# Performance work log

Hardware: AMD Instinct MI355X
Metric: run time of the kernel (lower is better)

The kernel has to match this reference:

```python
import jax, jax.numpy as jnp
import numpy as np

B, N, D = 2, 2048, 1024   # batch, seq_len, d_model
E = 2 * D                  # d_inner = d_model * expand_factor
F = 4 * D                  # ffn hidden
CHUNK = 128
EPS_LN = 1e-5


def setup_inputs() -> dict:
    key = jax.random.key(0)
    ks = jax.random.split(key, 16)
    s = 0.02
    return {
        "x": jax.random.normal(ks[0], (B, N, D), dtype=jnp.float32),
        # linear-attention projections (stored [in, out])
        "q_w": jax.random.normal(ks[1], (D, E), dtype=jnp.float32) * s,
        "q_b": jnp.zeros((E,), jnp.float32),
        "k_w": jax.random.normal(ks[2], (D, E), dtype=jnp.float32) * s,
        "k_b": jnp.zeros((E,), jnp.float32),
        "v_w": jax.random.normal(ks[3], (D, E), dtype=jnp.float32) * s,
        "v_b": jnp.zeros((E,), jnp.float32),
        "o_w": jax.random.normal(ks[4], (E, D), dtype=jnp.float32) * s,
        "o_b": jnp.zeros((D,), jnp.float32),
        # layer norms
        "ln1_g": jnp.ones((D,), jnp.float32), "ln1_b": jnp.zeros((D,), jnp.float32),
        "ln2_g": jnp.ones((D,), jnp.float32), "ln2_b": jnp.zeros((D,), jnp.float32),
        # ffn
        "w1": jax.random.normal(ks[5], (D, F), dtype=jnp.float32) * s,
        "b1": jnp.zeros((F,), jnp.float32),
        "w2": jax.random.normal(ks[6], (F, D), dtype=jnp.float32) * s,
        "b2": jnp.zeros((D,), jnp.float32),
    }


def _layer_norm(x, g, b):
    mu = jnp.mean(x, axis=-1, keepdims=True)
    var = jnp.mean(jnp.square(x - mu), axis=-1, keepdims=True)
    return (x - mu) * jax.lax.rsqrt(var + EPS_LN) * g + b


def _feature_map(x):
    return jax.nn.elu(x) + 1.0  # positive features


def _causal_linear_attention(Q, K, V):
    """Exactly cumsum(k v^T) formulation, computed chunk-recurrently.
    Q,K: [B,N,E] (post feature map), V: [B,N,E]. Returns [B,N,E]."""
    nC = N // CHUNK
    Qc = Q.reshape(B, nC, CHUNK, E).transpose(1, 0, 2, 3)
    Kc = K.reshape(B, nC, CHUNK, E).transpose(1, 0, 2, 3)
    Vc = V.reshape(B, nC, CHUNK, E).transpose(1, 0, 2, 3)
    tril = jnp.tril(jnp.ones((CHUNK, CHUNK), Q.dtype))

    def step(S, qkv):  # S: [B,E,E] running sum of k v^T
        q, k, v = qkv
        scores = jnp.einsum('bcd,bkd->bck', q, k) * tril  # intra-chunk causal
        intra = jnp.einsum('bck,bke->bce', scores, v)
        inter = jnp.einsum('bcd,bde->bce', q, S)
        S = S + jnp.einsum('bcd,bce->bde', k, v)
        return S, intra + inter

    S0 = jnp.zeros((B, E, E), Q.dtype)
    _, num = jax.lax.scan(step, S0, (Qc, Kc, Vc))  # [nC,B,CHUNK,E]
    num = num.transpose(1, 0, 2, 3).reshape(B, N, E)
    Z = jnp.cumsum(K, axis=1)                       # [B,N,E]
    den = jnp.einsum('bnd,bnd->bn', Q, Z)[..., None] + 1e-6
    return num / den


def reference(x, q_w, q_b, k_w, k_b, v_w, v_b, o_w, o_b,
              ln1_g, ln1_b, ln2_g, ln2_b, w1, b1, w2, b2):
    # training branch of SSDFLUIDLayer (linear attention), dropout = identity (eval)
    xn = _layer_norm(x, ln1_g, ln1_b)
    Q = _feature_map(xn @ q_w + q_b)
    K = _feature_map(xn @ k_w + k_b)
    V = xn @ v_w + v_b
    attn = _causal_linear_attention(Q, K, V) @ o_w + o_b
    x = x + attn
    xn2 = _layer_norm(x, ln2_g, ln2_b)
    ffn = jax.nn.gelu(xn2 @ w1 + b1, approximate=False) @ w2 + b2
    return x + ffn
```

## Files before the change

kernel.cpp:

```cpp
#include <hip/hip_runtime.h>
#include <math.h>

typedef unsigned short u16;
typedef short s16x8 __attribute__((ext_vector_type(8)));
typedef float f32x4 __attribute__((ext_vector_type(4)));
typedef long long ll;

__device__ inline u16 f2bf(float f) {
    unsigned u = __float_as_uint(f);
    u += 0x7fffu + ((u >> 16) & 1u);
    return (u16)(u >> 16);
}
__device__ inline float bf2f(u16 h) { return __uint_as_float(((unsigned)h) << 16); }

__device__ __forceinline__ void glds16(const u16* g, u16* l) {
    __builtin_amdgcn_global_load_lds(
        (__attribute__((address_space(1))) void*)(void*)g,
        (__attribute__((address_space(3))) void*)l, 16, 0, 0);
}

__global__ __launch_bounds__(256) void ln_bf16(const float* __restrict__ x,
                                               const float* __restrict__ g,
                                               const float* __restrict__ b,
                                               u16* __restrict__ out, int D) {
    int row = blockIdx.x;
    const float* xr = x + (size_t)row * D;
    int t = threadIdx.x;
    float4 v = ((const float4*)xr)[t];
    float s = v.x + v.y + v.z + v.w;
    __shared__ float sm[4];
    #pragma unroll
    for (int o = 32; o > 0; o >>= 1) s += __shfl_down(s, o, 64);
    int lane = t & 63, wv = t >> 6;
    if (lane == 0) sm[wv] = s;
    __syncthreads();
    float mean = (sm[0] + sm[1] + sm[2] + sm[3]) * (1.0f / 1024.0f);
    float dx = v.x - mean, dy = v.y - mean, dz = v.z - mean, dw = v.w - mean;
    float s2 = dx * dx + dy * dy + dz * dz + dw * dw;
    __syncthreads();
    #pragma unroll
    for (int o = 32; o > 0; o >>= 1) s2 += __shfl_down(s2, o, 64);
    if (lane == 0) sm[wv] = s2;
    __syncthreads();
    float var = (sm[0] + sm[1] + sm[2] + sm[3]) * (1.0f / 1024.0f);
    float rstd = rsqrtf(var + 1e-5f);
    float4 gg = ((const float4*)g)[t], bb = ((const float4*)b)[t];
    ushort4 o4;
    o4.x = f2bf(dx * rstd * gg.x + bb.x);
    o4.y = f2bf(dy * rstd * gg.y + bb.y);
    o4.z = f2bf(dz * rstd * gg.z + bb.z);
    o4.w = f2bf(dw * rstd * gg.w + bb.w);
    ((ushort4*)(out + (size_t)row * D))[t] = o4;
}

__global__ __launch_bounds__(256) void combine_ln(
    const float* __restrict__ x, const float* __restrict__ p0,
    const float* __restrict__ p1, const float* __restrict__ ob,
    const float* __restrict__ g, const float* __restrict__ b,
    float* __restrict__ x2, u16* __restrict__ xn2) {
    int row = blockIdx.x;
    int t = threadIdx.x;
    size_t base = (size_t)row * 256;
    float4 v = ((const float4*)x)[base + t];
    float4 a0 = ((const float4*)p0)[base + t];
    float4 a1 = ((const float4*)p1)[base + t];
    float4 ob4 = ((const float4*)ob)[t];
    v.x += a0.x + a1.x + ob4.x;
    v.y += a0.y + a1.y + ob4.y;
    v.z += a0.z + a1.z + ob4.z;
    v.w += a0.w + a1.w + ob4.w;
    ((float4*)x2)[base + t] = v;
    float s = v.x + v.y + v.z + v.w;
    __shared__ float sm[4];
    #pragma unroll
    for (int o = 32; o > 0; o >>= 1) s += __shfl_down(s, o, 64);
    int lane = t & 63, wv = t >> 6;
    if (lane == 0) sm[wv] = s;
    __syncthreads();
    float mean = (sm[0] + sm[1] + sm[2] + sm[3]) * (1.0f / 1024.0f);
    float dx = v.x - mean, dy = v.y - mean, dz = v.z - mean, dw = v.w - mean;
    float s2 = dx * dx + dy * dy + dz * dz + dw * dw;
    __syncthreads();
    #pragma unroll
    for (int o = 32; o > 0; o >>= 1) s2 += __shfl_down(s2, o, 64);
    if (lane == 0) sm[wv] = s2;
    __syncthreads();
    float var = (sm[0] + sm[1] + sm[2] + sm[3]) * (1.0f / 1024.0f);
    float rstd = rsqrtf(var + 1e-5f);
    float4 gg = ((const float4*)g)[t], bb = ((const float4*)b)[t];
    ushort4 o4;
    o4.x = f2bf(dx * rstd * gg.x + bb.x);
    o4.y = f2bf(dy * rstd * gg.y + bb.y);
    o4.z = f2bf(dz * rstd * gg.z + bb.z);
    o4.w = f2bf(dw * rstd * gg.w + bb.w);
    ((ushort4*)(xn2 + (size_t)row * 1024))[t] = o4;
}

__global__ __launch_bounds__(256) void combine_out(
    const float* __restrict__ x2, const float* __restrict__ p0,
    const float* __restrict__ p1, const float* __restrict__ b2,
    float* __restrict__ out) {
    size_t i = (size_t)blockIdx.x * 256 + threadIdx.x;
    int col4 = (int)(i & 255);
    float4 v = ((const float4*)x2)[i];
    float4 a0 = ((const float4*)p0)[i];
    float4 a1 = ((const float4*)p1)[i];
    float4 bb = ((const float4*)b2)[col4];
    v.x += a0.x + a1.x + bb.x;
    v.y += a0.y + a1.y + bb.y;
    v.z += a0.z + a1.z + bb.z;
    v.w += a0.w + a1.w + bb.w;
    ((float4*)out)[i] = v;
}

__global__ void prep(const float* __restrict__ qb, const float* __restrict__ kb,
                     const float* __restrict__ vb, float* __restrict__ bcat,
                     float* __restrict__ den, int E, int BN) {
    int i = blockIdx.x * 256 + threadIdx.x;
    if (i < E) {
        bcat[i] = qb[i];
        bcat[E + i] = kb[i];
        bcat[2 * E + i] = vb[i];
    }
    if (i < BN) den[i] = 0.f;
}

__global__ __launch_bounds__(256) void transpose_all(
    const float* __restrict__ q_w, const float* __restrict__ k_w,
    const float* __restrict__ v_w, const float* __restrict__ o_w,
    const float* __restrict__ w1, const float* __restrict__ w2,
    u16* __restrict__ qkvT, u16* __restrict__ oT,
    u16* __restrict__ w1T, u16* __restrict__ w2T) {
    int z = blockIdx.y;
    const float* src;
    u16* dst;
    int R, C, tprLog;
    switch (z) {
        case 0: src = q_w; dst = qkvT;                           R = 1024; C = 2048; tprLog = 6; break;
        case 1: src = k_w; dst = qkvT + (size_t)2 * 1024 * 1024; R = 1024; C = 2048; tprLog = 6; break;
        case 2: src = v_w; dst = qkvT + (size_t)4 * 1024 * 1024; R = 1024; C = 2048; tprLog = 6; break;
        case 3: src = o_w; dst = oT;                             R = 2048; C = 1024; tprLog = 5; break;
        case 4: src = w1;  dst = w1T;                            R = 1024; C = 4096; tprLog = 7; break;
        default: src = w2; dst = w2T;                            R = 4096; C = 1024; tprLog = 5; break;
    }
    int bx = blockIdx.x;
    int ntiles = (R >> 5) << (tprLog);
    if (bx >= ntiles) return;
    int c0 = (bx & ((1 << tprLog) - 1)) * 32;
    int r0 = (bx >> tprLog) * 32;
    __shared__ u16 tile[32][33];
    int tx = threadIdx.x & 31, ty = threadIdx.x >> 5;
    #pragma unroll
    for (int i = 0; i < 32; i += 8)
        tile[ty + i][tx] = f2bf(src[(size_t)(r0 + ty + i) * C + c0 + tx]);
    __syncthreads();
    #pragma unroll
    for (int i = 0; i < 32; i += 8)
        dst[(size_t)(c0 + ty + i) * R + r0 + tx] = tile[tx][ty + i];
}

__global__ __launch_bounds__(256) void transpose_u16(const u16* __restrict__ in,
                                                     u16* __restrict__ out,
                                                     int R, int C, int ldIn,
                                                     ll sIn, ll sOut) {
    in += (size_t)blockIdx.z * sIn;
    out += (size_t)blockIdx.z * sOut;
    __shared__ u16 tile[32][33];
    int tx = threadIdx.x & 31, ty = threadIdx.x >> 5;
    int c0 = blockIdx.x * 32, r0 = blockIdx.y * 32;
    #pragma unroll
    for (int i = 0; i < 32; i += 8)
        tile[ty + i][tx] = in[(size_t)(r0 + ty + i) * ldIn + c0 + tx];
    __syncthreads();
    #pragma unroll
    for (int i = 0; i < 32; i += 8)
        out[(size_t)(c0 + ty + i) * R + r0 + tx] = tile[tx][ty + i];
}

enum { EPI_QKV = 0, EPI_TRIL = 2, EPI_DIV = 3, EPI_GELU = 5, EPI_PART = 6 };

#define TM 128
#define TN 128

template <int EPI, int BKt>
__global__ __launch_bounds__(256) void gemm_nt(
    const u16* __restrict__ A, const u16* __restrict__ B, void* __restrict__ Cv,
    const float* __restrict__ bias, float* __restrict__ den,
    int M, int N, int K, int lda, int ldb,
    ll sA, ll sB, ll sC, ll sAux) {
    int z = blockIdx.z;
    A += (size_t)z * sA;
    B += (size_t)z * sB;

    int p = blockIdx.y * gridDim.x + blockIdx.x;
    int m0, n0;
    if (EPI == EPI_TRIL || EPI == EPI_DIV) {
        int nb = gridDim.x;
        int panel = nb * 4;
        int pp = p / panel, rr = p - pp * panel;
        m0 = (pp * 4 + (rr & 3)) * TM;
        n0 = (rr >> 2) * TN;
    } else {
        int g = p & 7, r = p >> 3;
        int lw = gridDim.x >> 2, lh = gridDim.y >> 1;
        int ly = r / lw, lx = r - ly * lw;
        m0 = ((g >> 2) * lh + ly) * TM;
        n0 = ((g & 3) * lw + lx) * TN;
    }

    int t = threadIdx.x;

    if (EPI == EPI_TRIL && n0 > m0 + (TM - 1)) {
        u16* C = (u16*)Cv + (size_t)z * sC;
        #pragma unroll
        for (int s = 0; s < 8; ++s) {
            int v = t + 256 * s;
            int row = v >> 4, cf = (v & 15) * 8;
            *(uint4*)&C[(size_t)(m0 + row) * N + n0 + cf] = make_uint4(0, 0, 0, 0);
        }
        return;
    }

    __shared__ __align__(16) u16 As[TM * BKt];
    __shared__ __align__(16) u16 Bs[TN * BKt];

    f32x4 acc[4][4];
    #pragma unroll
    for (int i = 0; i < 4; i++)
        #pragma unroll
        for (int j = 0; j < 4; j++) { f32x4 zz = {0.f, 0.f, 0.f, 0.f}; acc[i][j] = zz; }

    int kend = (EPI == EPI_DIV) ? (m0 + TM < K ? m0 + TM : K) : K;

    int lane = t & 63, wv = t >> 6;
    int lr = lane & 15, q = lane >> 4;
    int wm = (wv & 1) * 64, wn = (wv >> 1) * 64;

    u16* lA = As + wv * 32 * BKt;
    u16* lB = Bs + wv * 32 * BKt;

    int srow, skf;
    if (BKt == 32) {
        srow = wv * 32 + (lane >> 2);
        skf = (((lane & 3) - ((lane >> 3) & 3)) & 3) * 8;
    } else {
        srow = wv * 32 + (lane >> 3);
        skf = (((lane & 7) - (lane >> 3)) & 7) * 8;
    }
    const u16* gA0 = A + (size_t)(m0 + srow) * lda + skf;
    const u16* gB0 = B + (size_t)(n0 + srow) * ldb + skf;

    int ca[2][4], cb[2][4];
    #pragma unroll
    for (int i = 0; i < 4; i++) {
        int ra = wm + i * 16 + lr;
        int rb = wn + i * 16 + lr;
        if (BKt == 32) {
            ca[0][i] = (ra * 4 + ((q + (ra >> 1)) & 3)) * 8;
            cb[0][i] = (rb * 4 + ((q + (rb >> 1)) & 3)) * 8;
        } else {
            ca[0][i] = (ra * 8 + ((q + (ra & 7)) & 7)) * 8;
            ca[1][i] = (ra * 8 + ((4 + q + (ra & 7)) & 7)) * 8;
            cb[0][i] = (rb * 8 + ((q + (rb & 7)) & 7)) * 8;
            cb[1][i] = (rb * 8 + ((4 + q + (rb & 7)) & 7)) * 8;
        }
    }

    for (int k0 = 0; k0 < kend; k0 += BKt) {
        if (BKt == 32) {
            glds16(gA0 + k0, lA);
            glds16(gA0 + k0 + (size_t)16 * lda, lA + 16 * BKt);
            glds16(gB0 + k0, lB);
            glds16(gB0 + k0 + (size_t)16 * ldb, lB + 16 * BKt);
        } else {
            #pragma unroll
            for (int r = 0; r < 4; ++r) {
                glds16(gA0 + k0 + (size_t)(8 * r) * lda, lA + r * 8 * BKt);
                glds16(gB0 + k0 + (size_t)(8 * r) * ldb, lB + r * 8 * BKt);
            }
        }
        __syncthreads();
        #pragma unroll
        for (int kk = 0; kk < BKt / 32; ++kk) {
            s16x8 af[4], bfr[4];
            #pragma unroll
            for (int i = 0; i < 4; i++) af[i] = *(const s16x8*)&As[ca[kk][i]];
            #pragma unroll
            for (int j = 0; j < 4; j++) bfr[j] = *(const s16x8*)&Bs[cb[kk][j]];
            #pragma unroll
            for (int i = 0; i < 4; i++)
                #pragma unroll
                for (int j = 0; j < 4; j++)
                    acc[i][j] = __builtin_amdgcn_mfma_f32_16x16x32_bf16(af[i], bfr[j], acc[i][j], 0, 0, 0);
        }
        __syncthreads();
    }

    u16* Cb = (u16*)Cv + (size_t)z * sC;
    float* Cf = (float*)Cv + (size_t)z * sC;
    bool isQK = (EPI == EPI_QKV) && (n0 < 4096);
    #pragma unroll
    for (int i = 0; i < 4; i++) {
        #pragma unroll
        for (int r = 0; r < 4; r++) {
            int row = m0 + wm + i * 16 + q * 4 + r;
            float rs = 0.f;
            #pragma unroll
            for (int j = 0; j < 4; j++) {
                int col = n0 + wn + j * 16 + lr;
                float v = acc[i][j][r];
                if (EPI == EPI_QKV) {
                    v += bias[col];
                    if (isQK) v = (v > 0.f) ? (v + 1.f) : __expf(v);
                    Cb[(size_t)row * N + col] = f2bf(v);
                } else if (EPI == EPI_TRIL) {
                    v = (col <= row) ? v : 0.f;
                    rs += v;
                    Cb[(size_t)row * N + col] = f2bf(v);
                } else if (EPI == EPI_DIV) {
                    float d = den[(size_t)z * sAux + row] + 1e-6f;
                    Cb[(size_t)row * N + col] = f2bf(v / d);
                } else if (EPI == EPI_GELU) {
                    v += bias[col];
                    float u = v * (0.7978845608f + 0.0356774081f * v * v);
                    u = fminf(u, 40.f);
                    float e = __expf(2.f * u);
                    v = v * __fdividef(e, e + 1.f);
                    Cb[(size_t)row * N + col] = f2bf(v);
                } else if (EPI == EPI_PART) {
                    Cf[(size_t)row * N + col] = v;
                }
            }
            if (EPI == EPI_TRIL) {
                #pragma unroll
                for (int m = 1; m < 16; m <<= 1) rs += __shfl_xor(rs, m, 16);
                if (lr == 0) atomicAdd(&den[(size_t)z * sAux + row], rs);
            }
        }
    }
}

template <int EPI>
__global__ __launch_bounds__(512, 2) void gemm3b(
    const u16* __restrict__ A, const u16* __restrict__ B, u16* __restrict__ C,
    const float* __restrict__ bias, int M, int N, int K, int lda, int ldb) {

    __shared__ __align__(16) u16 lds[3][24576];

    int p = blockIdx.y * gridDim.x + blockIdx.x;
    int g = p & 7, rr = p >> 3;
    int lw = gridDim.x >> 2, lh = gridDim.y >> 1;
    int ly = rr / lw, lx = rr - ly * lw;
    int m0 = ((g >> 2) * lh + ly) * 128;
    int n0 = ((g & 3) * lw + lx) * 256;

    int t = threadIdx.x;
    int lane = t & 63, wid = t >> 6;
    int lr = lane & 15, q = lane >> 4;

    int skf = (((lane & 7) - (lane >> 3)) & 7) * 8;
    const u16* gA = A + (size_t)(m0 + wid * 16 + (lane >> 3)) * lda + skf;
    const u16* gB = B + (size_t)(n0 + wid * 32 + (lane >> 3)) * ldb + skf;
    int sdA = wid * 1024;
    int sdB = 8192 + wid * 2048;

    int nk = K >> 6;

    auto stageA = [&](int tt, int d) {
        int kt = (tt < nk ? tt : nk - 1) << 6;
        glds16(gA + kt, &lds[d][sdA]);
        glds16(gA + kt + (size_t)8 * lda, &lds[d][sdA + 512]);
    };
    auto stageB = [&](int tt, int d) {
        int kt = (tt < nk ? tt : nk - 1) << 6;
        #pragma unroll
        for (int r2 = 0; r2 < 4; ++r2)
            glds16(gB + kt + (size_t)(8 * r2) * ldb, &lds[d][sdB + r2 * 512]);
    };

    f32x4 acc[4][4];
    #pragma unroll
    for (int i = 0; i < 4; i++)
        #pragma unroll
        for (int j = 0; j < 4; j++) { f32x4 zz = {0.f, 0.f, 0.f, 0.f}; acc[i][j] = zz; }

    int wm = (wid >> 2) * 64, wn = (wid & 3) * 64;
    int aoff0 = wm * 64 + lr * 64 + (((q + lr) & 7) << 3);
    int aoff1 = wm * 64 + lr * 64 + (((4 + q + lr) & 7) << 3);
    int boff0 = 8192 + wn * 64 + lr * 64 + (((q + lr) & 7) << 3);
    int boff1 = 8192 + wn * 64 + lr * 64 + (((4 + q + lr) & 7) << 3);

    stageA(0, 0); stageB(0, 0);
    stageA(1, 1); stageB(1, 1);
    asm volatile("s_waitcnt vmcnt(6)" ::: "memory");
    asm volatile("s_barrier" ::: "memory");

    s16x8 a[4][2], b[4][2];

    int cur = 0;
    for (int tt = 0; tt < nk; ++tt) {
        int nx2 = cur + 2; if (nx2 >= 3) nx2 -= 3;
        const u16* L = &lds[cur][0];

        #pragma unroll
        for (int j = 0; j < 2; j++) {
            b[j][0] = *(const s16x8*)&L[boff0 + j * 1024];
            b[j][1] = *(const s16x8*)&L[boff1 + j * 1024];
        }
        #pragma unroll
        for (int i = 0; i < 4; i++) {
            a[i][0] = *(const s16x8*)&L[aoff0 + i * 1024];
            a[i][1] = *(const s16x8*)&L[aoff1 + i * 1024];
        }
        stageB(tt + 2, nx2);
        asm volatile("s_barrier" ::: "memory");
        __builtin_amdgcn_s_setprio(1);
        #pragma unroll
        for (int i = 0; i < 4; i++)
            #pragma unroll
            for (int j = 0; j < 2; j++) {
                acc[i][j] = __builtin_amdgcn_mfma_f32_16x16x32_bf16(a[i][0], b[j][0], acc[i][j], 0, 0, 0);
                acc[i][j] = __builtin_amdgcn_mfma_f32_16x16x32_bf16(a[i][1], b[j][1], acc[i][j], 0, 0, 0);
            }
        __builtin_amdgcn_s_setprio(0);
        asm volatile("s_barrier" ::: "memory");

        #pragma unroll
        for (int j = 2; j < 4; j++) {
            b[j][0] = *(const s16x8*)&L[boff0 + j * 1024];
            b[j][1] = *(const s16x8*)&L[boff1 + j * 1024];
        }
        stageA(tt + 2, nx2);
        asm volatile("s_barrier" ::: "memory");
        __builtin_amdgcn_s_setprio(1);
        #pragma unroll
        for (int i = 0; i < 4; i++)
            #pragma unroll
            for (int j = 2; j < 4; j++) {
                acc[i][j] = __builtin_amdgcn_mfma_f32_16x16x32_bf16(a[i][0], b[j][0], acc[i][j], 0, 0, 0);
                acc[i][j] = __builtin_amdgcn_mfma_f32_16x16x32_bf16(a[i][1], b[j][1], acc[i][j], 0, 0, 0);
            }
        __builtin_amdgcn_s_setprio(0);
        asm volatile("s_waitcnt vmcnt(6)" ::: "memory");
        asm volatile("s_barrier" ::: "memory");

        cur = cur + 1; if (cur >= 3) cur -= 3;
    }

    asm volatile("s_waitcnt vmcnt(0)" ::: "memory");

    #pragma unroll
    for (int i = 0; i < 4; i++) {
        #pragma unroll
        for (int r = 0; r < 4; r++) {
            int row = m0 + wm + i * 16 + q * 4 + r;
            #pragma unroll
            for (int j = 0; j < 4; j++) {
                int col = n0 + wn + j * 16 + lr;
                float v = acc[i][j][r] + bias[col];
                if (EPI == EPI_QKV) {
                    if (n0 + wn + j * 16 < 4096) v = (v > 0.f) ? (v + 1.f) : __expf(v);
                } else {
                    float u = v * (0.7978845608f + 0.0356774081f * v * v);
                    u = fminf(u, 40.f);
                    float e = __expf(2.f * u);
                    v = v * __fdividef(e, e + 1.f);
                }
                C[(size_t)row * N + col] = f2bf(v);
            }
        }
    }
}

extern "C" void kernel_launch(void* const* d_in, const int* in_sizes, int n_in,
                              void* d_out, int out_size, void* d_ws, size_t ws_size,
                              hipStream_t stream) {
    const float* x    = (const float*)d_in[0];
    const float* q_w  = (const float*)d_in[1];
    const float* q_b  = (const float*)d_in[2];
    const float* k_w  = (const float*)d_in[3];
    const float* k_b  = (const float*)d_in[4];
    const float* v_w  = (const float*)d_in[5];
    const float* v_b  = (const float*)d_in[6];
    const float* o_w  = (const float*)d_in[7];
    const float* o_b  = (const float*)d_in[8];
    const float* ln1g = (const float*)d_in[9];
    const float* ln1b = (const float*)d_in[10];
    const float* ln2g = (const float*)d_in[11];
    const float* ln2b = (const float*)d_in[12];
    const float* w1   = (const float*)d_in[13];
    const float* b1   = (const float*)d_in[14];
    const float* w2   = (const float*)d_in[15];
    const float* b2   = (const float*)d_in[16];
    float* out = (float*)d_out;

    constexpr int Bb = 2, N = 2048, D = 1024, E = 2048, F = 4096;
    constexpr int BN = Bb * N;
    constexpr int E3 = 3 * E;

    char* ws = (char*)d_ws;
    size_t off = 0;
    auto alloc = [&](size_t bytes) -> void* {
        void* p = ws + off;
        off += (bytes + 255) & ~(size_t)255;
        return p;
    };
    u16*   qkvT = (u16*)alloc((size_t)E3 * D * 2);
    u16*   oT   = (u16*)alloc((size_t)D * E * 2);
    u16*   w1T  = (u16*)alloc((size_t)F * D * 2);
    u16*   w2T  = (u16*)alloc((size_t)D * F * 2);
    float* bcat = (float*)alloc((size_t)E3 * 4);
    u16*   xn   = (u16*)alloc((size_t)BN * D * 2);
    u16*   QKV  = (u16*)alloc((size_t)BN * E3 * 2);
    u16*   Vt   = (u16*)alloc((size_t)Bb * E * N * 2);
    u16*   Amat = (u16*)alloc((size_t)Bb * N * N * 2);
    float* den  = (float*)alloc((size_t)BN * 4);

    u16*   xn2 = xn;
    u16*   P   = QKV;
    u16*   h   = QKV + (size_t)8 * 1024 * 1024;
    float* x2  = (float*)Vt;
    float* pt0 = (float*)Amat;
    float* pt1 = pt0 + (size_t)BN * D;

    dim3 blk(256);

    prep<<<dim3((BN + 255) / 256), blk, 0, stream>>>(q_b, k_b, v_b, bcat, den, E, BN);

    transpose_all<<<dim3(4096, 6), blk, 0, stream>>>(
        q_w, k_w, v_w, o_w, w1, w2, qkvT, oT, w1T, w2T);

    ln_bf16<<<BN, blk, 0, stream>>>(x, ln1g, ln1b, xn, D);

    gemm3b<EPI_QKV><<<dim3(E3 / 256, BN / 128), dim3(512), 0, stream>>>(
        xn, qkvT, QKV, bcat, BN, E3, D, D, D);

    transpose_u16<<<dim3(E / 32, N / 32, Bb), blk, 0, stream>>>(
        QKV + 2 * E, Vt, N, E, E3, (ll)N * E3, (ll)E * N);

    gemm_nt<EPI_TRIL, 64><<<dim3(N / 128, N / 128, Bb), blk, 0, stream>>>(
        QKV, QKV + E, Amat, nullptr, den, N, N, E, E3, E3,
        (ll)N * E3, (ll)N * E3, (ll)N * N, (ll)N);

    gemm_nt<EPI_DIV, 64><<<dim3(E / 128, N / 128, Bb), blk, 0, stream>>>(
        Amat, Vt, P, nullptr, den, N, E, N, N, N,
        (ll)N * N, (ll)E * N, (ll)N * E, (ll)N);

    gemm_nt<EPI_PART, 64><<<dim3(D / 128, BN / 128, 2), blk, 0, stream>>>(
        P, oT, pt0, nullptr, nullptr, BN, D, E / 2, E, E,
        (ll)(E / 2), (ll)(E / 2), (ll)BN * D, 0);

    combine_ln<<<BN, blk, 0, stream>>>(x, pt0, pt1, o_b, ln2g, ln2b, x2, xn2);

    gemm3b<EPI_GELU><<<dim3(F / 256, BN / 128), dim3(512), 0, stream>>>(
        xn2, w1T, h, b1, BN, F, D, D, D);

    gemm_nt<EPI_PART, 64><<<dim3(D / 128, BN / 128, 2), blk, 0, stream>>>(
        h, w2T, pt0, nullptr, nullptr, BN, D, F / 2, F, F,
        (ll)(F / 2), (ll)(F / 2), (ll)BN * D, 0);

    combine_out<<<dim3(BN * D / 4 / 256), blk, 0, stream>>>(x2, pt0, pt1, b2, out);
}
```

Baseline: 459.7 us.

## Rework bf16 GEMM into 256-thread blocks with 64x128 wave tiles

Replaces the 512-thread, 8-wave GEMM used for the QKV and FFN-up projections with a 256-thread, 4-wave version. Each wave now computes a 64x128 output tile, and the K step per stage drops from 64 to 32. The aim is more register-level reuse of the A and B fragments per wave and half the shared-memory footprint per stage. The XOR-style LDS swizzle is removed in favour of a plain 32-element row layout, which risks LDS bank conflicts. The larger accumulator array per thread may also raise register pressure.

```diff
diff --git a/kernel.cpp b/kernel.cpp
--- a/kernel.cpp
+++ b/kernel.cpp
@@ -341,11 +341,11 @@
 }
 
 template <int EPI>
-__global__ __launch_bounds__(512, 2) void gemm3b(
+__global__ __launch_bounds__(256, 2) void gemm2b(
     const u16* __restrict__ A, const u16* __restrict__ B, u16* __restrict__ C,
     const float* __restrict__ bias, int M, int N, int K, int lda, int ldb) {
 
-    __shared__ __align__(16) u16 lds[3][24576];
+    __shared__ __align__(16) u16 lds[3][12288];
 
     int p = blockIdx.y * gridDim.x + blockIdx.x;
     int g = p & 7, rr = p >> 3;
@@ -358,44 +358,41 @@
     int lane = t & 63, wid = t >> 6;
     int lr = lane & 15, q = lane >> 4;
 
-    int skf = (((lane & 7) - (lane >> 3)) & 7) * 8;
-    const u16* gA = A + (size_t)(m0 + wid * 16 + (lane >> 3)) * lda + skf;
-    const u16* gB = B + (size_t)(n0 + wid * 32 + (lane >> 3)) * ldb + skf;
+    const u16* gA = A + (size_t)(m0 + wid * 32 + (lane >> 2)) * lda + (lane & 3) * 8;
+    const u16* gB = B + (size_t)(n0 + wid * 64 + (lane >> 2)) * ldb + (lane & 3) * 8;
     int sdA = wid * 1024;
-    int sdB = 8192 + wid * 2048;
-
-    int nk = K >> 6;
+    int sdB = 4096 + wid * 2048;
+
+    int nk = K >> 5;
 
     auto stageA = [&](int tt, int d) {
-        int kt = (tt < nk ? tt : nk - 1) << 6;
+        int kt = (tt < nk ? tt : nk - 1) << 5;
         glds16(gA + kt, &lds[d][sdA]);
-        glds16(gA + kt + (size_t)8 * lda, &lds[d][sdA + 512]);
+        glds16(gA + kt + (size_t)16 * lda, &lds[d][sdA + 512]);
     };
     auto stageB = [&](int tt, int d) {
-        int kt = (tt < nk ? tt : nk - 1) << 6;
+        int kt = (tt < nk ? tt : nk - 1) << 5;
         #pragma unroll
         for (int r2 = 0; r2 < 4; ++r2)
-            glds16(gB + kt + (size_t)(8 * r2) * ldb, &lds[d][sdB + r2 * 512]);
+            glds16(gB + kt + (size_t)(16 * r2) * ldb, &lds[d][sdB + r2 * 512]);
     };
 
-    f32x4 acc[4][4];
+    f32x4 acc[4][8];
     #pragma unroll
     for (int i = 0; i < 4; i++)
         #pragma unroll
-        for (int j = 0; j < 4; j++) { f32x4 zz = {0.f, 0.f, 0.f, 0.f}; acc[i][j] = zz; }
-
-    int wm = (wid >> 2) * 64, wn = (wid & 3) * 64;
-    int aoff0 = wm * 64 + lr * 64 + (((q + lr) & 7) << 3);
-    int aoff1 = wm * 64 + lr * 64 + (((4 + q + lr) & 7) << 3);
-    int boff0 = 8192 + wn * 64 + lr * 64 + (((q + lr) & 7) << 3);
-    int boff1 = 8192 + wn * 64 + lr * 64 + (((4 + q + lr) & 7) << 3);
+        for (int j = 0; j < 8; j++) { f32x4 zz = {0.f, 0.f, 0.f, 0.f}; acc[i][j] = zz; }
+
+    int wm = (wid & 1) * 64, wn = (wid >> 1) * 128;
+    int aoff = (wm + lr) * 32 + q * 8;
+    int boff = 4096 + (wn + lr) * 32 + q * 8;
 
     stageA(0, 0); stageB(0, 0);
     stageA(1, 1); stageB(1, 1);
     asm volatile("s_waitcnt vmcnt(6)" ::: "memory");
     asm volatile("s_barrier" ::: "memory");
 
-    s16x8 a[4][2], b[4][2];
+    s16x8 af[4], bf_[8];
 
     int cur = 0;
     for (int tt = 0; tt < nk; ++tt) {
@@ -403,43 +400,30 @@
         const u16* L = &lds[cur][0];
 
         #pragma unroll
-        for (int j = 0; j < 2; j++) {
-            b[j][0] = *(const s16x8*)&L[boff0 + j * 1024];
-            b[j][1] = *(const s16x8*)&L[boff1 + j * 1024];
-        }
-        #pragma unroll
-        for (int i = 0; i < 4; i++) {
-            a[i][0] = *(const s16x8*)&L[aoff0 + i * 1024];
-            a[i][1] = *(const s16x8*)&L[aoff1 + i * 1024];
-        }
+        for (int j = 0; j < 4; j++) bf_[j] = *(const s16x8*)&L[boff + j * 512];
+        #pragma unroll
+        for (int i = 0; i < 4; i++) af[i] = *(const s16x8*)&L[aoff + i * 512];
         stageB(tt + 2, nx2);
         asm volatile("s_barrier" ::: "memory");
         __builtin_amdgcn_s_setprio(1);
         #pragma unroll
         for (int i = 0; i < 4; i++)
             #pragma unroll
-            for (int j = 0; j < 2; j++) {
-                acc[i][j] = __builtin_amdgcn_mfma_f32_16x16x32_bf16(a[i][0], b[j][0], acc[i][j], 0, 0, 0);
-                acc[i][j] = __builtin_amdgcn_mfma_f32_16x16x32_bf16(a[i][1], b[j][1], acc[i][j], 0, 0, 0);
-            }
+            for (int j = 0; j < 4; j++)
+                acc[i][j] = __builtin_amdgcn_mfma_f32_16x16x32_bf16(af[i], bf_[j], acc[i][j], 0, 0, 0);
         __builtin_amdgcn_s_setprio(0);
         asm volatile("s_barrier" ::: "memory");
 
         #pragma unroll
-        for (int j = 2; j < 4; j++) {
-            b[j][0] = *(const s16x8*)&L[boff0 + j * 1024];
-            b[j][1] = *(const s16x8*)&L[boff1 + j * 1024];
-        }
+        for (int j = 4; j < 8; j++) bf_[j] = *(const s16x8*)&L[boff + j * 512];
         stageA(tt + 2, nx2);
         asm volatile("s_barrier" ::: "memory");
         __builtin_amdgcn_s_setprio(1);
         #pragma unroll
         for (int i = 0; i < 4; i++)
             #pragma unroll
-            for (int j = 2; j < 4; j++) {
-                acc[i][j] = __builtin_amdgcn_mfma_f32_16x16x32_bf16(a[i][0], b[j][0], acc[i][j], 0, 0, 0);
-                acc[i][j] = __builtin_amdgcn_mfma_f32_16x16x32_bf16(a[i][1], b[j][1], acc[i][j], 0, 0, 0);
-            }
+            for (int j = 4; j < 8; j++)
+                acc[i][j] = __builtin_amdgcn_mfma_f32_16x16x32_bf16(af[i], bf_[j], acc[i][j], 0, 0, 0);
         __builtin_amdgcn_s_setprio(0);
         asm volatile("s_waitcnt vmcnt(6)" ::: "memory");
         asm volatile("s_barrier" ::: "memory");
@@ -455,7 +439,7 @@
         for (int r = 0; r < 4; r++) {
             int row = m0 + wm + i * 16 + q * 4 + r;
             #pragma unroll
-            for (int j = 0; j < 4; j++) {
+            for (int j = 0; j < 8; j++) {
                 int col = n0 + wn + j * 16 + lr;
                 float v = acc[i][j][r] + bias[col];
                 if (EPI == EPI_QKV) {
@@ -532,7 +516,7 @@
 
     ln_bf16<<<BN, blk, 0, stream>>>(x, ln1g, ln1b, xn, D);
 
-    gemm3b<EPI_QKV><<<dim3(E3 / 256, BN / 128), dim3(512), 0, stream>>>(
+    gemm2b<EPI_QKV><<<dim3(E3 / 256, BN / 128), blk, 0, stream>>>(
         xn, qkvT, QKV, bcat, BN, E3, D, D, D);
 
     transpose_u16<<<dim3(E / 32, N / 32, Bb), blk, 0, stream>>>(
@@ -552,7 +536,7 @@
 
     combine_ln<<<BN, blk, 0, stream>>>(x, pt0, pt1, o_b, ln2g, ln2b, x2, xn2);
 
-    gemm3b<EPI_GELU><<<dim3(F / 256, BN / 128), dim3(512), 0, stream>>>(
+    gemm2b<EPI_GELU><<<dim3(F / 256, BN / 128), blk, 0, stream>>>(
         xn2, w1T, h, b1, BN, F, D, D, D);
 
     gemm_nt<EPI_PART, 64><<<dim3(D / 128, BN / 128, 2), blk, 0, stream>>>(
```

After: 454.8 us. Within noise of the previous version (-1.1%).
